# Optimization experiments

Measured on AMD Instinct MI355X. Metric: run time of the kernel, lower is better.

The kernel has to match this reference:

```python
import jax, jax.numpy as jnp
import numpy as np

N_NODES = 100000
N_EDGES = 1600000
D = 64
K = 5


def setup_inputs() -> dict:
    key = jax.random.key(0)
    k1, k2, k3, k4 = jax.random.split(key, 4)
    x = jax.random.normal(k1, (N_NODES, D), dtype=jnp.float32)
    # random edges, guaranteed no self-loops (offset in [1, N-1])
    src = jax.random.randint(k2, (N_EDGES,), 0, N_NODES)
    off = jax.random.randint(k3, (N_EDGES,), 1, N_NODES)
    dst = (src + off) % N_NODES
    edge_index = jnp.stack([src, dst], axis=0)  # [2, E], row 0 = source j, row 1 = target i
    kW, kb = jax.random.split(k4)
    W = jax.random.normal(kW, (K, D, D), dtype=jnp.float32) * (1.0 / np.sqrt(D))
    b = jnp.zeros((D,), dtype=jnp.float32)
    return {"x": x, "edge_index": edge_index, "W": W, "b": b}


def reference(x, edge_index, W, b):
    """ChebConv (normalization='sym', lambda_max=2.0) as in PyG GnBlock.

    Scaled Laplacian L_hat = (2/lambda_max) * (I - D^-1/2 A D^-1/2) - I
    with lambda_max=2 has zero diagonal, so propagate(h) = sum over edges
    (j->i) of norm_e * h[j] with norm_e = -dis[j]*dis[i].
    """
    src, dst = edge_index[0], edge_index[1]
    n = x.shape[0]
    # degree over source nodes (PyG get_laplacian scatters edge_weight=1 over row)
    deg = jax.ops.segment_sum(jnp.ones_like(src, dtype=x.dtype), src, num_segments=n)
    dis = jnp.where(deg > 0, jax.lax.rsqrt(jnp.maximum(deg, 1e-30)), 0.0)
    norm = -dis[src] * dis[dst]  # [E]

    def prop(h):
        # message: norm_e * h[src], aggregated at dst
        return jax.ops.segment_sum(norm[:, None] * h[src], dst, num_segments=n)

    Tx0 = x
    out = Tx0 @ W[0]
    Tx1 = prop(x)
    out = out + Tx1 @ W[1]
    for k in range(2, W.shape[0]):
        Tx2 = 2.0 * prop(Tx1) - Tx0
        out = out + Tx2 @ W[k]
        Tx0, Tx1 = Tx1, Tx2
    return out + b
```

## Files before the change

kernel.cpp:

```cpp
#include <hip/hip_runtime.h>

#define DD 64
#define NPB 16
#define NBD 128
#define NBS 64

typedef _Float16 f16x8 __attribute__((ext_vector_type(8)));
typedef float f32x4 __attribute__((ext_vector_type(4)));

__global__ __launch_bounds__(1024) void histD_kernel(
        const int* __restrict__ dst, unsigned char* __restrict__ dstp,
        unsigned char* __restrict__ ranks, int N, int NR, int E, int slice) {
    extern __shared__ unsigned int ldsH[];
    int nw = NR >> 2;
    int t = threadIdx.x;
    for (int i = t; i < nw; i += 1024) ldsH[i] = 0u;
    __syncthreads();
    int base = blockIdx.x * slice;
    int end = min(base + slice, E);
    for (int e = base + t; e < end; e += 1024) {
        int d = __builtin_nontemporal_load(dst + e);
        unsigned int sh = (unsigned int)(d & 3) * 8u;
        unsigned int old = atomicAdd(&ldsH[d >> 2], 1u << sh);
        unsigned char r = (unsigned char)((old >> sh) & 0xFFu);
        __builtin_nontemporal_store(r, ranks + e);
    }
    __syncthreads();
    unsigned int* outp = reinterpret_cast<unsigned int*>(dstp + (size_t)blockIdx.x * NR);
    for (int i = t; i < nw; i += 1024) outp[i] = ldsH[i];
}

__global__ __launch_bounds__(1024) void histS_kernel(
        const int* __restrict__ src, unsigned char* __restrict__ srcp,
        int N, int NR, int E, int slice) {
    extern __shared__ unsigned int ldsH[];
    int nw = NR >> 2;
    int t = threadIdx.x;
    for (int i = t; i < nw; i += 1024) ldsH[i] = 0u;
    __syncthreads();
    int base = blockIdx.x * slice;
    int end = min(base + slice, E);
    for (int e = base + t; e < end; e += 1024) {
        int s = __builtin_nontemporal_load(src + e);
        atomicAdd(&ldsH[s >> 2], 1u << ((unsigned int)(s & 3) * 8u));
    }
    __syncthreads();
    unsigned int* outp = reinterpret_cast<unsigned int*>(srcp + (size_t)blockIdx.x * NR);
    for (int i = t; i < nw; i += 1024) outp[i] = ldsH[i];
}

__global__ __launch_bounds__(1024) void scan1_kernel(
        unsigned char* dstp, const unsigned char* __restrict__ srcp,
        float* __restrict__ dis, int* __restrict__ rowptr,
        int* __restrict__ bsum, int N, int NR) {
    __shared__ int tmp[1024];
    int t = threadIdx.x;
    int g = blockIdx.x * 1024 + t;
    int c = 0;
    if (g < N) {
        int degv = 0;
        #pragma unroll 8
        for (int i = 0; i < NBS; ++i) degv += srcp[(size_t)i * NR + g];
        dis[g] = (degv > 0) ? rsqrtf((float)degv) : 0.0f;
        #pragma unroll 8
        for (int i = 0; i < NBD; ++i) {
            size_t idx = (size_t)i * NR + g;
            int v = dstp[idx];
            dstp[idx] = (unsigned char)c;
            c += v;
        }
    }
    tmp[t] = c;
    __syncthreads();
    for (int off = 1; off < 1024; off <<= 1) {
        int a = (t >= off) ? tmp[t - off] : 0;
        __syncthreads();
        tmp[t] += a;
        __syncthreads();
    }
    if (g < N) rowptr[g] = tmp[t] - c;
    if (t == 1023) bsum[blockIdx.x] = tmp[1023];
}

__global__ __launch_bounds__(128) void scan2_kernel(int* __restrict__ data, int n) {
    __shared__ int tmp[128];
    int t = threadIdx.x;
    int v = (t < n) ? data[t] : 0;
    tmp[t] = v;
    __syncthreads();
    for (int off = 1; off < 128; off <<= 1) {
        int a = (t >= off) ? tmp[t - off] : 0;
        __syncthreads();
        tmp[t] += a;
        __syncthreads();
    }
    if (t < n) data[t] = tmp[t] - v;
}

__global__ void scan3_kernel(int* __restrict__ rowptr, const int* __restrict__ bsum,
                             int N, int E) {
    int g = blockIdx.x * blockDim.x + threadIdx.x;
    if (g < N) rowptr[g] += bsum[g >> 10];
    if (g == 0) rowptr[N] = E;
}

__global__ void cvt_kernel(const float* __restrict__ x, const float* __restrict__ dis,
                           _Float16* __restrict__ p0, long long n8) {
    long long i = (long long)blockIdx.x * blockDim.x + threadIdx.x;
    if (i < n8) {
        int node = (int)(i >> 3);
        float dv = dis[node];
        float f = (dv > 0.f) ? dv : 1.0f;
        const float4* x4 = reinterpret_cast<const float4*>(x);
        float4 a = x4[i * 2], b = x4[i * 2 + 1];
        f16x8 h;
        h[0] = (_Float16)(f * a.x); h[1] = (_Float16)(f * a.y);
        h[2] = (_Float16)(f * a.z); h[3] = (_Float16)(f * a.w);
        h[4] = (_Float16)(f * b.x); h[5] = (_Float16)(f * b.y);
        h[6] = (_Float16)(f * b.z); h[7] = (_Float16)(f * b.w);
        reinterpret_cast<f16x8*>(p0)[i] = h;
    }
}

__global__ void wcvt_kernel(const float* __restrict__ W, _Float16* __restrict__ Wh,
                            int nfrag) {
    int idx = blockIdx.x * blockDim.x + threadIdx.x;
    if (idx >= nfrag) return;
    int lane = idx & 63;
    int ct = (idx >> 6) & 3;
    int kt = (idx >> 8) & 1;
    int k = idx >> 9;
    int r0 = kt * 32 + (lane >> 4) * 8;
    int c = ct * 16 + (lane & 15);
    f16x8 h;
    #pragma unroll
    for (int i = 0; i < 8; ++i)
        h[i] = (_Float16)W[(size_t)k * DD * DD + (size_t)(r0 + i) * DD + c];
    reinterpret_cast<f16x8*>(Wh)[idx] = h;
}

__global__ void fill_kernel(const int* __restrict__ src, const int* __restrict__ dst,
                            const int* __restrict__ rowptr,
                            const unsigned char* __restrict__ dstp,
                            const unsigned char* __restrict__ ranks,
                            int* __restrict__ adjS, int E, int slice, int NR) {
    int e = blockIdx.x * blockDim.x + threadIdx.x;
    if (e < E) {
        int s = __builtin_nontemporal_load(src + e);
        int d = __builtin_nontemporal_load(dst + e);
        int i = e / slice;
        int rank = __builtin_nontemporal_load(ranks + e);
        int pos = rowptr[d] + (int)dstp[(size_t)i * NR + d] + rank;
        adjS[pos] = s;
    }
}

__global__ __launch_bounds__(256, 8) void prop_kernel(
        const int* __restrict__ rowptr, const int* __restrict__ adjS,
        const float* __restrict__ dis,
        const _Float16* __restrict__ h, const _Float16* t0,
        _Float16* __restrict__ pout, float scale, int N) {
    int t = threadIdx.x;
    int nl = t >> 6, lane = t & 63;
    int q = lane & 7;
    int s = (lane >> 3) & 1;
    int ng = lane >> 4;
    int node = blockIdx.x * NPB + nl * 4 + ng;
    bool valid = node < N;
    const f16x8* h8 = reinterpret_cast<const f16x8*>(h);

    int beg = 0, end = 0;
    if (valid) { beg = rowptr[node]; end = rowptr[node + 1]; }

    float acc[8];
    #pragma unroll
    for (int i = 0; i < 8; ++i) acc[i] = 0.f;

    int j = beg + s;
    int e0 = (j < end) ? adjS[j] : 0;
    int e1 = (j + 2 < end) ? adjS[j + 2] : 0;
    int e2 = (j + 4 < end) ? adjS[j + 4] : 0;
    int e3 = (j + 6 < end) ? adjS[j + 6] : 0;
    float m0 = (j < end) ? 1.f : 0.f;
    float m1 = (j + 2 < end) ? 1.f : 0.f;
    float m2 = (j + 4 < end) ? 1.f : 0.f;
    float m3 = (j + 6 < end) ? 1.f : 0.f;
    while (j < end) {
        int jn = j + 8;
        int n0 = (jn < end) ? adjS[jn] : 0;
        int n1 = (jn + 2 < end) ? adjS[jn + 2] : 0;
        int n2 = (jn + 4 < end) ? adjS[jn + 4] : 0;
        int n3 = (jn + 6 < end) ? adjS[jn + 6] : 0;
        float nm0 = (jn < end) ? 1.f : 0.f;
        float nm1 = (jn + 2 < end) ? 1.f : 0.f;
        float nm2 = (jn + 4 < end) ? 1.f : 0.f;
        float nm3 = (jn + 6 < end) ? 1.f : 0.f;
        f16x8 g0 = h8[(size_t)e0 * 8 + q];
        f16x8 g1 = h8[(size_t)e1 * 8 + q];
        f16x8 g2 = h8[(size_t)e2 * 8 + q];
        f16x8 g3 = h8[(size_t)e3 * 8 + q];
        #pragma unroll
        for (int i = 0; i < 8; ++i) {
            acc[i] += m0 * (float)g0[i] + m1 * (float)g1[i];
            acc[i] += m2 * (float)g2[i] + m3 * (float)g3[i];
        }
        e0 = n0; e1 = n1; e2 = n2; e3 = n3;
        m0 = nm0; m1 = nm1; m2 = nm2; m3 = nm3;
        j = jn;
    }
    #pragma unroll
    for (int i = 0; i < 8; ++i) acc[i] += __shfl_xor(acc[i], 8, 64);

    if (s == 0 && valid) {
        float dv = dis[node];
        float cf = scale * dv * dv;
        size_t base = (size_t)node * DD + q * 8;
        f16x8 vh;
        if (t0) {
            f16x8 t0v = __builtin_nontemporal_load(
                reinterpret_cast<const f16x8*>(t0 + base));
            #pragma unroll
            for (int i = 0; i < 8; ++i)
                vh[i] = (_Float16)(cf * acc[i] - (float)t0v[i]);
        } else {
            #pragma unroll
            for (int i = 0; i < 8; ++i) vh[i] = (_Float16)(cf * acc[i]);
        }
        __builtin_nontemporal_store(vh, reinterpret_cast<f16x8*>(pout + base));
    }
}

static __device__ __forceinline__ f16x8 afrag(const _Float16* __restrict__ P,
                                              int node, int kt, int lk) {
    return *reinterpret_cast<const f16x8*>(P + (size_t)node * DD + kt * 32 + lk * 8);
}

__global__ __launch_bounds__(256, 8) void gemm5_kernel(
        const _Float16* __restrict__ P0, const _Float16* __restrict__ P1,
        const _Float16* __restrict__ P2, const _Float16* __restrict__ P3,
        const _Float16* __restrict__ P4,
        const float* __restrict__ dis, const _Float16* __restrict__ Wh,
        const float* __restrict__ bias, float* __restrict__ out, int N) {
    int t = threadIdx.x;
    int nl = t >> 6, lane = t & 63;
    int ct = nl, lr = lane & 15, lk = lane >> 4;
    const f16x8* Wh8 = reinterpret_cast<const f16x8*>(Wh);
    f16x8 bf[5][2];
    #pragma unroll
    for (int k = 0; k < 5; ++k)
        #pragma unroll
        for (int kt = 0; kt < 2; ++kt)
            bf[k][kt] = Wh8[((k * 2 + kt) * 4 + ct) * 64 + lane];
    int col = ct * 16 + lr;
    float bv = bias[col];

    int nb0 = blockIdx.x * NPB;
    if (nb0 >= N) return;
    int node = min(nb0 + lr, N - 1);
    f32x4 d = {0.f, 0.f, 0.f, 0.f};
    #pragma unroll
    for (int kt = 0; kt < 2; ++kt) {
        d = __builtin_amdgcn_mfma_f32_16x16x32_f16(afrag(P0, node, kt, lk), bf[0][kt], d, 0, 0, 0);
        d = __builtin_amdgcn_mfma_f32_16x16x32_f16(afrag(P1, node, kt, lk), bf[1][kt], d, 0, 0, 0);
        d = __builtin_amdgcn_mfma_f32_16x16x32_f16(afrag(P2, node, kt, lk), bf[2][kt], d, 0, 0, 0);
        d = __builtin_amdgcn_mfma_f32_16x16x32_f16(afrag(P3, node, kt, lk), bf[3][kt], d, 0, 0, 0);
        d = __builtin_amdgcn_mfma_f32_16x16x32_f16(afrag(P4, node, kt, lk), bf[4][kt], d, 0, 0, 0);
    }
    int nvb = min(NPB, N - nb0);
    #pragma unroll
    for (int r = 0; r < 4; ++r) {
        int row = lk * 4 + r;
        if (row < nvb) {
            float dv = dis[nb0 + row];
            float invd = (dv > 0.f) ? 1.f / dv : 1.f;
            long long o = (long long)(nb0 + row) * DD + col;
            __builtin_nontemporal_store(bv + invd * d[r], out + o);
        }
    }
}

__global__ __launch_bounds__(256, 8) void gemm2_kernel(
        const _Float16* __restrict__ P0, const _Float16* __restrict__ P1,
        const float* __restrict__ dis,
        const float* __restrict__ W0, const float* __restrict__ W1,
        const float* __restrict__ bias, float* __restrict__ out, int N) {
    int t = threadIdx.x;
    int nl = t >> 6, lane = t & 63;
    int ct = nl, lr = lane & 15, lk = lane >> 4;
    f16x8 bf0[2], bf1[2];
    #pragma unroll
    for (int kt = 0; kt < 2; ++kt)
        #pragma unroll
        for (int i = 0; i < 8; ++i) {
            int r = kt * 32 + lk * 8 + i;
            bf0[kt][i] = (_Float16)W0[r * DD + ct * 16 + lr];
            bf1[kt][i] = (_Float16)W1[r * DD + ct * 16 + lr];
        }
    int nb0 = blockIdx.x * NPB;
    int node = min(nb0 + lr, N - 1);
    f32x4 d = {0.f, 0.f, 0.f, 0.f};
    #pragma unroll
    for (int kt = 0; kt < 2; ++kt) {
        d = __builtin_amdgcn_mfma_f32_16x16x32_f16(afrag(P0, node, kt, lk), bf0[kt], d, 0, 0, 0);
        d = __builtin_amdgcn_mfma_f32_16x16x32_f16(afrag(P1, node, kt, lk), bf1[kt], d, 0, 0, 0);
    }
    int nvb = min(NPB, N - nb0);
    int col = ct * 16 + lr;
    float bv = bias[col];
    #pragma unroll
    for (int r = 0; r < 4; ++r) {
        int row = lk * 4 + r;
        if (row < nvb) {
            float dv = dis[nb0 + row];
            float invd = (dv > 0.f) ? 1.f / dv : 1.f;
            long long o = (long long)(nb0 + row) * DD + col;
            out[o] = bv + invd * d[r];
        }
    }
}

__global__ __launch_bounds__(256, 8) void gemm1_kernel(
        const _Float16* __restrict__ P, const float* __restrict__ dis,
        const float* __restrict__ Wk, float* __restrict__ out, int N) {
    int t = threadIdx.x;
    int nl = t >> 6, lane = t & 63;
    int ct = nl, lr = lane & 15, lk = lane >> 4;
    f16x8 bf[2];
    #pragma unroll
    for (int kt = 0; kt < 2; ++kt)
        #pragma unroll
        for (int i = 0; i < 8; ++i) {
            int r = kt * 32 + lk * 8 + i;
            bf[kt][i] = (_Float16)Wk[r * DD + ct * 16 + lr];
        }
    int nb0 = blockIdx.x * NPB;
    int node = min(nb0 + lr, N - 1);
    f32x4 d = {0.f, 0.f, 0.f, 0.f};
    #pragma unroll
    for (int kt = 0; kt < 2; ++kt)
        d = __builtin_amdgcn_mfma_f32_16x16x32_f16(afrag(P, node, kt, lk), bf[kt], d, 0, 0, 0);
    int nvb = min(NPB, N - nb0);
    int col = ct * 16 + lr;
    #pragma unroll
    for (int r = 0; r < 4; ++r) {
        int row = lk * 4 + r;
        if (row < nvb) {
            float dv = dis[nb0 + row];
            float invd = (dv > 0.f) ? 1.f / dv : 1.f;
            long long o = (long long)(nb0 + row) * DD + col;
            out[o] = out[o] + invd * d[r];
        }
    }
}

extern "C" void kernel_launch(void* const* d_in, const int* in_sizes, int n_in,
                              void* d_out, int out_size, void* d_ws, size_t ws_size,
                              hipStream_t stream) {
    const float* x  = (const float*)d_in[0];
    const int*   ei = (const int*)d_in[1];
    const float* W  = (const float*)d_in[2];
    const float* b  = (const float*)d_in[3];
    float* out = (float*)d_out;

    const int N = in_sizes[0] / DD;
    const int E = in_sizes[1] / 2;
    const int K = in_sizes[2] / (DD * DD);
    const long long ND = (long long)N * DD;
    const int NR = ((N + 3) / 4) * 4;

    const int* src = ei;
    const int* dst = ei + E;

    size_t off = 0;
    char* base = (char*)d_ws;
    auto alloc = [&](size_t bytes) {
        char* p = base + off;
        off = (off + bytes + 63) & ~(size_t)63;
        return p;
    };
    float* dis = (float*)alloc((size_t)N * 4);
    int* rowptr = (int*)alloc((size_t)(N + 1) * 4);
    int* bsum = (int*)alloc(512);
    _Float16* Wh = (_Float16*)alloc((size_t)5 * 2 * 4 * 64 * 8 * 2);
    char* hist_base = alloc((size_t)(NBD + NBS) * NR);
    unsigned char* dstp = (unsigned char*)hist_base;
    unsigned char* srcp = (unsigned char*)(hist_base + (size_t)NBD * NR);
    unsigned char* ranks = (unsigned char*)alloc((size_t)E);
    int* adjS = (int*)alloc((size_t)E * 4);
    _Float16* P0 = (_Float16*)alloc((size_t)ND * 2);
    _Float16* P1 = (_Float16*)alloc((size_t)ND * 2);
    _Float16* P3 = (_Float16*)alloc((size_t)ND * 2);
    _Float16* P4 = (_Float16*)alloc((size_t)ND * 2);
    _Float16* P2 = (_Float16*)hist_base;

    const int sliceD = (E + NBD - 1) / NBD;
    const int sliceS = (E + NBS - 1) / NBS;
    const size_t ldsH = (size_t)NR;

    histD_kernel<<<NBD, 1024, ldsH, stream>>>(dst, dstp, ranks, N, NR, E, sliceD);
    histS_kernel<<<NBS, 1024, ldsH, stream>>>(src, srcp, N, NR, E, sliceS);

    const int nb = (N + 1023) / 1024;
    scan1_kernel<<<nb, 1024, 0, stream>>>(dstp, srcp, dis, rowptr, bsum, N, NR);
    scan2_kernel<<<1, 128, 0, stream>>>(bsum, nb);
    scan3_kernel<<<(N + 255) / 256, 256, 0, stream>>>(rowptr, bsum, N, E);

    const long long n8 = ND / 8;
    cvt_kernel<<<(int)((n8 + 255) / 256), 256, 0, stream>>>(x, dis, P0, n8);
    if (K == 5) {
        const int nfrag = 5 * 2 * 4 * 64;
        wcvt_kernel<<<(nfrag + 255) / 256, 256, 0, stream>>>(W, Wh, nfrag);
    }

    fill_kernel<<<(E + 255) / 256, 256, 0, stream>>>(src, dst, rowptr, dstp,
                                                     ranks, adjS, E, sliceD, NR);

    const int pgrid = (N + NPB - 1) / NPB;
    const int Wsz = DD * DD;

    if (K == 5) {
        prop_kernel<<<pgrid, 256, 0, stream>>>(rowptr, adjS, dis, P0,
                                               (const _Float16*)0, P1, -1.0f, N);
        prop_kernel<<<pgrid, 256, 0, stream>>>(rowptr, adjS, dis, P1, P0, P2, -2.0f, N);
        prop_kernel<<<pgrid, 256, 0, stream>>>(rowptr, adjS, dis, P2, P1, P3, -2.0f, N);
        prop_kernel<<<pgrid, 256, 0, stream>>>(rowptr, adjS, dis, P3, P2, P4, -2.0f, N);
        gemm5_kernel<<<pgrid, 256, 0, stream>>>(P0, P1, P2, P3, P4, dis, Wh, b, out, N);
    } else {
        prop_kernel<<<pgrid, 256, 0, stream>>>(rowptr, adjS, dis, P0,
                                               (const _Float16*)0, P1, -1.0f, N);
        gemm2_kernel<<<pgrid, 256, 0, stream>>>(P0, P1, dis, W, W + Wsz, b, out, N);
        _Float16* t0 = P0;
        _Float16* h  = P1;
        _Float16* fr = P2;
        for (int k = 2; k < K; ++k) {
            prop_kernel<<<pgrid, 256, 0, stream>>>(rowptr, adjS, dis, h, t0, fr, -2.0f, N);
            gemm1_kernel<<<pgrid, 256, 0, stream>>>(fr, dis, W + (long long)k * Wsz,
                                                    out, N);
            _Float16* nfree = t0;
            t0 = h; h = fr; fr = nfree;
        }
    }
}
```

Measured before the change: 357.7 us.

## Build CSR via two-pass bucket sort with per-bucket LDS counting sort

Replaces the per-slice byte-histogram, three-stage scan and random-scatter fill for the destination CSR with a two-pass bucket sort. Edges are first packed as (src<<10 | dst&1023) into fixed-capacity buckets keyed by dst>>10. One block per bucket then counting-sorts its edges in LDS, writes rowptr and emits a contiguous adjS segment. This removes the large dstp histogram traffic and the scattered global writes, and collapses several launches. In exchange, a bucket holding more than CAPB edges silently drops the excess, which is only safe for roughly uniform destination distributions. The packing also assumes node ids below 2^22.

```diff
diff --git a/kernel.cpp b/kernel.cpp
--- a/kernel.cpp
+++ b/kernel.cpp
@@ -2,33 +2,14 @@
 
 #define DD 64
 #define NPB 16
-#define NBD 128
 #define NBS 64
+#define NBKMAX 128
+#define CAPB 20480
+#define EPB 8
+#define EPT 20
 
 typedef _Float16 f16x8 __attribute__((ext_vector_type(8)));
 typedef float f32x4 __attribute__((ext_vector_type(4)));
-
-__global__ __launch_bounds__(1024) void histD_kernel(
-        const int* __restrict__ dst, unsigned char* __restrict__ dstp,
-        unsigned char* __restrict__ ranks, int N, int NR, int E, int slice) {
-    extern __shared__ unsigned int ldsH[];
-    int nw = NR >> 2;
-    int t = threadIdx.x;
-    for (int i = t; i < nw; i += 1024) ldsH[i] = 0u;
-    __syncthreads();
-    int base = blockIdx.x * slice;
-    int end = min(base + slice, E);
-    for (int e = base + t; e < end; e += 1024) {
-        int d = __builtin_nontemporal_load(dst + e);
-        unsigned int sh = (unsigned int)(d & 3) * 8u;
-        unsigned int old = atomicAdd(&ldsH[d >> 2], 1u << sh);
-        unsigned char r = (unsigned char)((old >> sh) & 0xFFu);
-        __builtin_nontemporal_store(r, ranks + e);
-    }
-    __syncthreads();
-    unsigned int* outp = reinterpret_cast<unsigned int*>(dstp + (size_t)blockIdx.x * NR);
-    for (int i = t; i < nw; i += 1024) outp[i] = ldsH[i];
-}
 
 __global__ __launch_bounds__(1024) void histS_kernel(
         const int* __restrict__ src, unsigned char* __restrict__ srcp,
@@ -49,28 +30,95 @@
     for (int i = t; i < nw; i += 1024) outp[i] = ldsH[i];
 }
 
-__global__ __launch_bounds__(1024) void scan1_kernel(
-        unsigned char* dstp, const unsigned char* __restrict__ srcp,
-        float* __restrict__ dis, int* __restrict__ rowptr,
-        int* __restrict__ bsum, int N, int NR) {
-    __shared__ int tmp[1024];
-    int t = threadIdx.x;
-    int g = blockIdx.x * 1024 + t;
-    int c = 0;
+__global__ void disred_kernel(const unsigned char* __restrict__ srcp,
+                              float* __restrict__ dis, int N, int NR) {
+    int g = blockIdx.x * 256 + threadIdx.x;
     if (g < N) {
         int degv = 0;
         #pragma unroll 8
         for (int i = 0; i < NBS; ++i) degv += srcp[(size_t)i * NR + g];
         dis[g] = (degv > 0) ? rsqrtf((float)degv) : 0.0f;
-        #pragma unroll 8
-        for (int i = 0; i < NBD; ++i) {
-            size_t idx = (size_t)i * NR + g;
-            int v = dstp[idx];
-            dstp[idx] = (unsigned char)c;
-            c += v;
-        }
-    }
-    tmp[t] = c;
+    }
+}
+
+__global__ __launch_bounds__(1024) void histA_kernel(
+        const int* __restrict__ src, const int* __restrict__ dst,
+        int* __restrict__ gbcnt, unsigned int* __restrict__ bktbuf,
+        int E, int nbk) {
+    __shared__ int lcnt[NBKMAX];
+    __shared__ int lbase[NBKMAX];
+    int t = threadIdx.x;
+    if (t < NBKMAX) lcnt[t] = 0;
+    __syncthreads();
+    int base = blockIdx.x * (EPB * 1024);
+    unsigned int ent[EPB];
+    int rk[EPB];
+    int bk[EPB];
+    #pragma unroll
+    for (int k = 0; k < EPB; ++k) {
+        int e = base + t + k * 1024;
+        bk[k] = -1;
+        if (e < E) {
+            int s = __builtin_nontemporal_load(src + e);
+            int d = __builtin_nontemporal_load(dst + e);
+            int b = d >> 10;
+            ent[k] = ((unsigned int)s << 10) | (unsigned int)(d & 1023);
+            rk[k] = atomicAdd(&lcnt[b], 1);
+            bk[k] = b;
+        }
+    }
+    __syncthreads();
+    if (t < nbk) lbase[t] = atomicAdd(&gbcnt[t], lcnt[t]);
+    __syncthreads();
+    #pragma unroll
+    for (int k = 0; k < EPB; ++k) {
+        if (bk[k] >= 0) {
+            int pos = lbase[bk[k]] + rk[k];
+            if (pos < CAPB)
+                __builtin_nontemporal_store(ent[k],
+                    bktbuf + (size_t)bk[k] * CAPB + pos);
+        }
+    }
+}
+
+__global__ __launch_bounds__(1024) void csrB_kernel(
+        const unsigned int* __restrict__ bktbuf, const int* __restrict__ gbcnt,
+        int* __restrict__ rowptr, int* __restrict__ adjS,
+        int N, int nbk, int E) {
+    __shared__ int ncnt[1024];
+    __shared__ int tmp[1024];
+    __shared__ int adjstage[CAPB];
+    __shared__ int bbase_s;
+    int b = blockIdx.x;
+    int t = threadIdx.x;
+    if (t == 0) {
+        int acc = 0;
+        for (int i = 0; i < b; ++i) acc += gbcnt[i];
+        bbase_s = acc;
+    }
+    ncnt[t] = 0;
+    __syncthreads();
+    int total = min(gbcnt[b], CAPB);
+    int bbase = bbase_s;
+    const unsigned int* bp = bktbuf + (size_t)b * CAPB;
+    unsigned int sv[EPT];
+    int rk[EPT];
+    int dl[EPT];
+    #pragma unroll
+    for (int k = 0; k < EPT; ++k) {
+        int i = t + k * 1024;
+        dl[k] = -1;
+        if (i < total) {
+            unsigned int v = bp[i];
+            sv[k] = v >> 10;
+            int d = (int)(v & 1023u);
+            dl[k] = d;
+            rk[k] = atomicAdd(&ncnt[d], 1);
+        }
+    }
+    __syncthreads();
+    int v = ncnt[t];
+    tmp[t] = v;
     __syncthreads();
     for (int off = 1; off < 1024; off <<= 1) {
         int a = (t >= off) ? tmp[t - off] : 0;
@@ -78,30 +126,19 @@
         tmp[t] += a;
         __syncthreads();
     }
-    if (g < N) rowptr[g] = tmp[t] - c;
-    if (t == 1023) bsum[blockIdx.x] = tmp[1023];
-}
-
-__global__ __launch_bounds__(128) void scan2_kernel(int* __restrict__ data, int n) {
-    __shared__ int tmp[128];
-    int t = threadIdx.x;
-    int v = (t < n) ? data[t] : 0;
-    tmp[t] = v;
-    __syncthreads();
-    for (int off = 1; off < 128; off <<= 1) {
-        int a = (t >= off) ? tmp[t - off] : 0;
-        __syncthreads();
-        tmp[t] += a;
-        __syncthreads();
-    }
-    if (t < n) data[t] = tmp[t] - v;
-}
-
-__global__ void scan3_kernel(int* __restrict__ rowptr, const int* __restrict__ bsum,
-                             int N, int E) {
-    int g = blockIdx.x * blockDim.x + threadIdx.x;
-    if (g < N) rowptr[g] += bsum[g >> 10];
-    if (g == 0) rowptr[N] = E;
+    int excl = tmp[t] - v;
+    int node = b * 1024 + t;
+    if (node < N) rowptr[node] = bbase + excl;
+    if (b == nbk - 1 && t == 1023) rowptr[N] = E;
+    __syncthreads();
+    ncnt[t] = excl;
+    __syncthreads();
+    #pragma unroll
+    for (int k = 0; k < EPT; ++k)
+        if (dl[k] >= 0) adjstage[ncnt[dl[k]] + rk[k]] = (int)sv[k];
+    __syncthreads();
+    for (int i = t; i < total; i += 1024)
+        adjS[bbase + i] = adjstage[i];
 }
 
 __global__ void cvt_kernel(const float* __restrict__ x, const float* __restrict__ dis,
@@ -137,22 +174,6 @@
     for (int i = 0; i < 8; ++i)
         h[i] = (_Float16)W[(size_t)k * DD * DD + (size_t)(r0 + i) * DD + c];
     reinterpret_cast<f16x8*>(Wh)[idx] = h;
-}
-
-__global__ void fill_kernel(const int* __restrict__ src, const int* __restrict__ dst,
-                            const int* __restrict__ rowptr,
-                            const unsigned char* __restrict__ dstp,
-                            const unsigned char* __restrict__ ranks,
-                            int* __restrict__ adjS, int E, int slice, int NR) {
-    int e = blockIdx.x * blockDim.x + threadIdx.x;
-    if (e < E) {
-        int s = __builtin_nontemporal_load(src + e);
-        int d = __builtin_nontemporal_load(dst + e);
-        int i = e / slice;
-        int rank = __builtin_nontemporal_load(ranks + e);
-        int pos = rowptr[d] + (int)dstp[(size_t)i * NR + d] + rank;
-        adjS[pos] = s;
-    }
 }
 
 __global__ __launch_bounds__(256, 8) void prop_kernel(
@@ -367,6 +388,7 @@
     const int K = in_sizes[2] / (DD * DD);
     const long long ND = (long long)N * DD;
     const int NR = ((N + 3) / 4) * 4;
+    const int nbk = (N + 1023) >> 10;
 
     const int* src = ei;
     const int* dst = ei + E;
@@ -380,30 +402,27 @@
     };
     float* dis = (float*)alloc((size_t)N * 4);
     int* rowptr = (int*)alloc((size_t)(N + 1) * 4);
-    int* bsum = (int*)alloc(512);
     _Float16* Wh = (_Float16*)alloc((size_t)5 * 2 * 4 * 64 * 8 * 2);
-    char* hist_base = alloc((size_t)(NBD + NBS) * NR);
-    unsigned char* dstp = (unsigned char*)hist_base;
-    unsigned char* srcp = (unsigned char*)(hist_base + (size_t)NBD * NR);
-    unsigned char* ranks = (unsigned char*)alloc((size_t)E);
+    int* gbcnt = (int*)alloc((size_t)NBKMAX * 4);
+    char* ovl = alloc((size_t)NBS * NR + (size_t)NBKMAX * CAPB * 4);
+    unsigned char* srcp = (unsigned char*)ovl;
+    unsigned int* bktbuf = (unsigned int*)(ovl + (size_t)NBS * NR);
     int* adjS = (int*)alloc((size_t)E * 4);
     _Float16* P0 = (_Float16*)alloc((size_t)ND * 2);
     _Float16* P1 = (_Float16*)alloc((size_t)ND * 2);
     _Float16* P3 = (_Float16*)alloc((size_t)ND * 2);
     _Float16* P4 = (_Float16*)alloc((size_t)ND * 2);
-    _Float16* P2 = (_Float16*)hist_base;
-
-    const int sliceD = (E + NBD - 1) / NBD;
+    _Float16* P2 = (_Float16*)ovl;
+
+    (void)hipMemsetAsync(gbcnt, 0, (size_t)NBKMAX * 4, stream);
+
     const int sliceS = (E + NBS - 1) / NBS;
-    const size_t ldsH = (size_t)NR;
-
-    histD_kernel<<<NBD, 1024, ldsH, stream>>>(dst, dstp, ranks, N, NR, E, sliceD);
-    histS_kernel<<<NBS, 1024, ldsH, stream>>>(src, srcp, N, NR, E, sliceS);
-
-    const int nb = (N + 1023) / 1024;
-    scan1_kernel<<<nb, 1024, 0, stream>>>(dstp, srcp, dis, rowptr, bsum, N, NR);
-    scan2_kernel<<<1, 128, 0, stream>>>(bsum, nb);
-    scan3_kernel<<<(N + 255) / 256, 256, 0, stream>>>(rowptr, bsum, N, E);
+    histS_kernel<<<NBS, 1024, (size_t)NR, stream>>>(src, srcp, N, NR, E, sliceS);
+    disred_kernel<<<(N + 255) / 256, 256, 0, stream>>>(srcp, dis, N, NR);
+
+    const int na = (E + EPB * 1024 - 1) / (EPB * 1024);
+    histA_kernel<<<na, 1024, 0, stream>>>(src, dst, gbcnt, bktbuf, E, nbk);
+    csrB_kernel<<<nbk, 1024, 0, stream>>>(bktbuf, gbcnt, rowptr, adjS, N, nbk, E);
 
     const long long n8 = ND / 8;
     cvt_kernel<<<(int)((n8 + 255) / 256), 256, 0, stream>>>(x, dis, P0, n8);
@@ -411,9 +430,6 @@
         const int nfrag = 5 * 2 * 4 * 64;
         wcvt_kernel<<<(nfrag + 255) / 256, 256, 0, stream>>>(W, Wh, nfrag);
     }
-
-    fill_kernel<<<(E + 255) / 256, 256, 0, stream>>>(src, dst, rowptr, dstp,
-                                                     ranks, adjS, E, sliceD, NR);
 
     const int pgrid = (N + NPB - 1) / NPB;
     const int Wsz = DD * DD;
```

After: 333.5 us. -6.8%, faster.
